# Kernel optimization log

Hardware: AMD Instinct MI355X
Metric: run time of the kernel (lower is better)

## Reference

```python
import jax, jax.numpy as jnp
import numpy as np

B = 128          # batch of independent QP instances
N = 512          # n_assets
N_ITERS = 500    # accelerated projected-gradient iterations (converges tightly)
POWER_ITERS = 30 # power iterations for Lipschitz estimate


def setup_inputs() -> dict:
    key = jax.random.key(0)
    k1, k2 = jax.random.split(key)
    mu = 0.1 * jax.random.normal(k1, (B, N), dtype=jnp.float32)
    # Sigma must be symmetric PSD for cp.quad_form to define a convex QP
    A = jax.random.normal(k2, (B, N, N), dtype=jnp.float32)
    Sigma = jnp.einsum('bik,bjk->bij', A, A) / N + 1e-3 * jnp.eye(N, dtype=jnp.float32)
    return {"mu": mu, "Sigma": Sigma}


def _project_simplex(v):
    # Euclidean projection of each row of v onto {w : sum w = 1, w >= 0}
    n = v.shape[-1]
    u = jnp.sort(v, axis=-1)[..., ::-1]                    # descending
    css = jnp.cumsum(u, axis=-1) - 1.0
    ind = jnp.arange(1, n + 1, dtype=v.dtype)
    rho = jnp.sum(u - css / ind > 0, axis=-1, keepdims=True)  # >= 1
    theta = jnp.take_along_axis(css, rho - 1, axis=-1) / rho.astype(v.dtype)
    return jnp.maximum(v - theta, 0.0)


def _solve_qp(mu, Sigma):
    # minimize w^T Sigma w - mu^T w  s.t.  sum w = 1, w >= 0
    Sigma = 0.5 * (Sigma + jnp.swapaxes(Sigma, -1, -2))  # quad_form assumes symmetric

    # Lipschitz constant of grad: 2*lambda_max(Sigma), via power iteration
    b = jnp.ones((Sigma.shape[0], Sigma.shape[-1]), dtype=mu.dtype) / Sigma.shape[-1]
    def power_step(b, _):
        Sb = jnp.einsum('bij,bj->bi', Sigma, b)
        b = Sb / (jnp.linalg.norm(Sb, axis=-1, keepdims=True) + 1e-12)
        return b, None
    b, _ = jax.lax.scan(power_step, b, None, length=POWER_ITERS)
    lmax = jnp.einsum('bi,bij,bj->b', b, Sigma, b)[:, None]  # [B,1]
    step = 1.0 / (2.0 * lmax + 1e-8)

    # Accelerated projected gradient (FISTA) on the simplex
    w0 = jnp.ones_like(mu) / mu.shape[-1]
    def fista_step(carry, _):
        w, y, t = carry
        g = 2.0 * jnp.einsum('bij,bj->bi', Sigma, y) - mu
        w_new = _project_simplex(y - step * g)
        t_new = 0.5 * (1.0 + jnp.sqrt(1.0 + 4.0 * t * t))
        y_new = w_new + ((t - 1.0) / t_new) * (w_new - w)
        return (w_new, y_new, t_new), None
    (w, _, _), _ = jax.lax.scan(fista_step, (w0, w0, jnp.float32(1.0)), None, length=N_ITERS)
    return w


def reference(mu, Sigma):
    return _solve_qp(mu, Sigma)
```

## Files before the change

### kernel.cpp

```cpp
#include <hip/hip_runtime.h>
#include <hip/hip_fp16.h>
#include <math.h>

#define BATCH 128
#define NDIM 512
#define NPAIR 256
#define POWER_ITERS 30
#define N_ITERS 500
#define REGK 16
#define LDSP 16
#define STRM 32

typedef _Float16 half2_t __attribute__((ext_vector_type(2)));

union H2x4 { float4 f4; half2_t h[4]; };

__device__ __forceinline__ float4 ld4(const float* p) { return *(const float4*)p; }
__device__ __forceinline__ float4 f4_add(float4 a, float4 b) {
  return make_float4(a.x + b.x, a.y + b.y, a.z + b.z, a.w + b.w);
}
__device__ __forceinline__ float wave_sum64(float x) {
#pragma unroll
  for (int off = 1; off < 64; off <<= 1) x += __shfl_xor(x, off, 64);
  return x;
}
__device__ __forceinline__ float wave_max64(float x) {
#pragma unroll
  for (int off = 1; off < 64; off <<= 1) x = fmaxf(x, __shfl_xor(x, off, 64));
  return x;
}
__device__ __forceinline__ void fd4(float4 sv, half2_t yy,
                                    float& a0, float& a1, float& a2, float& a3) {
  H2x4 s; s.f4 = sv;
  a0 = __builtin_amdgcn_fdot2(s.h[0], yy, a0, false);
  a1 = __builtin_amdgcn_fdot2(s.h[1], yy, a1, false);
  a2 = __builtin_amdgcn_fdot2(s.h[2], yy, a2, false);
  a3 = __builtin_amdgcn_fdot2(s.h[3], yy, a3, false);
}

__global__ void sym_conv_kernel(const float* __restrict__ S, half2_t* __restrict__ Sh) {
  const int bb = blockIdx.x, ti = blockIdx.y, tj = blockIdx.z;
  if (tj < ti) return;
  __shared__ float ta[32][33];
  __shared__ float tb[32][33];
  const float* base = S + (size_t)bb * NDIM * NDIM;
  half2_t* dst = Sh + (size_t)bb * NPAIR * NDIM;
  const int tx = threadIdx.x, ty = threadIdx.y;
#pragma unroll
  for (int k = 0; k < 4; k++) {
    int r = ty + 8 * k;
    ta[r][tx] = base[(size_t)(ti * 32 + r) * NDIM + tj * 32 + tx];
    tb[r][tx] = base[(size_t)(tj * 32 + r) * NDIM + ti * 32 + tx];
  }
  __syncthreads();
#pragma unroll
  for (int k = 0; k < 2; k++) {
    int pi = ty + 8 * k;
    float v0 = 0.5f * (ta[2 * pi][tx] + tb[tx][2 * pi]);
    float v1 = 0.5f * (ta[2 * pi + 1][tx] + tb[tx][2 * pi + 1]);
    half2_t o; o[0] = (_Float16)v0; o[1] = (_Float16)v1;
    dst[(size_t)(ti * 16 + pi) * NDIM + tj * 32 + tx] = o;
  }
  if (ti != tj) {
#pragma unroll
    for (int k = 0; k < 2; k++) {
      int pi = ty + 8 * k;
      float v0 = 0.5f * (tb[2 * pi][tx] + ta[tx][2 * pi]);
      float v1 = 0.5f * (tb[2 * pi + 1][tx] + ta[tx][2 * pi + 1]);
      half2_t o; o[0] = (_Float16)v0; o[1] = (_Float16)v1;
      dst[(size_t)(tj * 16 + pi) * NDIM + ti * 32 + tx] = o;
    }
  }
}

__device__ __forceinline__ void combine_z(const float* __restrict__ zsc, int lane, float* z8) {
#pragma unroll
  for (int q = 0; q < 2; q++) {
    float4 zz = ld4(zsc + 0 * NDIM + 8 * lane + 4 * q);
    zz = f4_add(zz, ld4(zsc + 1 * NDIM + 8 * lane + 4 * q));
    zz = f4_add(zz, ld4(zsc + 2 * NDIM + 8 * lane + 4 * q));
    zz = f4_add(zz, ld4(zsc + 3 * NDIM + 8 * lane + 4 * q));
    z8[4 * q + 0] = zz.x; z8[4 * q + 1] = zz.y;
    z8[4 * q + 2] = zz.z; z8[4 * q + 3] = zz.w;
  }
}

__device__ __forceinline__ void store_y_pairs(half2_t* ysh, int lane, const float* y8) {
  H2x4 yo;
#pragma unroll
  for (int q = 0; q < 4; q++) {
    half2_t v; v[0] = (_Float16)y8[2 * q]; v[1] = (_Float16)y8[2 * q + 1];
    yo.h[q] = v;
  }
  *(float4*)(ysh + 4 * lane) = yo.f4;
}

__global__ __launch_bounds__(512)
void qp_solver_h(const float* __restrict__ mu,
                 const half2_t* __restrict__ Sh,
                 float* __restrict__ out) {
  __shared__ __align__(16) float4 lsm[4 * LDSP][128];
  __shared__ __align__(16) half2_t yh2[NPAIR];
  __shared__ __align__(16) float zsc[4 * NDIM];
  __shared__ int stopf;
  const int tid = threadIdx.x;
  const int g = tid >> 7;
  const int c = tid & 127;
  const int b = blockIdx.x;
  const half2_t* Sb = Sh + (size_t)b * NPAIR * NDIM;
  const float invn = 1.0f / (float)NDIM;
  const half2_t* rp = Sb + (size_t)(64 * g) * NDIM + 4 * c;
  const half2_t* gp = rp + (size_t)(REGK + LDSP) * NDIM;

  float4 sreg[REGK];
#pragma unroll
  for (int p = 0; p < REGK; p++) sreg[p] = *(const float4*)(rp + (size_t)p * NDIM);
#pragma unroll
  for (int k = 0; k < LDSP; k++)
    lsm[g * LDSP + k][c] = *(const float4*)(rp + (size_t)(REGK + k) * NDIM);

  if (tid < NPAIR) { half2_t v; v[0] = (_Float16)invn; v[1] = (_Float16)invn; yh2[tid] = v; }
  if (tid == 0) stopf = 0;

  float y8[8], w8[8];
  float t = 1.0f, step = 0.f, maxinc = 0.f;
  float th = -3e38f;
  if (tid < 64) {
#pragma unroll
    for (int k = 0; k < 8; k++) { y8[k] = invn; w8[k] = invn; }
  }
  __syncthreads();

  const int TOT = POWER_ITERS + 1 + N_ITERS;
  for (int it = 0; it < TOT; it++) {
    float a0 = 0.f, a1 = 0.f, a2 = 0.f, a3 = 0.f;
    {
      const half2_t* ybase = yh2 + 64 * g;
      unsigned m = 0;
#pragma unroll
      for (int j = 0; j < 8; j++) {
        const uint4 u = *(const uint4*)(ybase + REGK + LDSP + 4 * j);
        m |= ((u.x | u.y | u.z | u.w) != 0u ? 1u : 0u) << j;
      }
      float4 stA[4], stB[4];
      if (m & 1u) {
#pragma unroll
        for (int k = 0; k < 4; k++) stA[k] = *(const float4*)(gp + (size_t)(0 + k) * NDIM);
      }
      if (m & 2u) {
#pragma unroll
        for (int k = 0; k < 4; k++) stB[k] = *(const float4*)(gp + (size_t)(4 + k) * NDIM);
      }
#pragma unroll
      for (int ch = 0; ch < REGK / 4; ch++) {
        H2x4 y4; y4.f4 = *(const float4*)(ybase + 4 * ch);
#pragma unroll
        for (int q = 0; q < 4; q++) fd4(sreg[4 * ch + q], y4.h[q], a0, a1, a2, a3);
      }
      if (m & 1u) {
        H2x4 y4; y4.f4 = *(const float4*)(ybase + REGK + LDSP + 0);
#pragma unroll
        for (int k = 0; k < 4; k++) fd4(stA[k], y4.h[k], a0, a1, a2, a3);
      }
      if (m & 4u) {
#pragma unroll
        for (int k = 0; k < 4; k++) stA[k] = *(const float4*)(gp + (size_t)(8 + k) * NDIM);
      }
#pragma unroll
      for (int ch = 0; ch < 2; ch++) {
        H2x4 y4; y4.f4 = *(const float4*)(ybase + REGK + 4 * ch);
#pragma unroll
        for (int q = 0; q < 4; q++)
          fd4(lsm[g * LDSP + 4 * ch + q][c], y4.h[q], a0, a1, a2, a3);
      }
      if (m & 2u) {
        H2x4 y4; y4.f4 = *(const float4*)(ybase + REGK + LDSP + 4);
#pragma unroll
        for (int k = 0; k < 4; k++) fd4(stB[k], y4.h[k], a0, a1, a2, a3);
      }
      if (m & 8u) {
#pragma unroll
        for (int k = 0; k < 4; k++) stB[k] = *(const float4*)(gp + (size_t)(12 + k) * NDIM);
      }
#pragma unroll
      for (int ch = 2; ch < 4; ch++) {
        H2x4 y4; y4.f4 = *(const float4*)(ybase + REGK + 4 * ch);
#pragma unroll
        for (int q = 0; q < 4; q++)
          fd4(lsm[g * LDSP + 4 * ch + q][c], y4.h[q], a0, a1, a2, a3);
      }
      if (m & 4u) {
        H2x4 y4; y4.f4 = *(const float4*)(ybase + REGK + LDSP + 8);
#pragma unroll
        for (int k = 0; k < 4; k++) fd4(stA[k], y4.h[k], a0, a1, a2, a3);
      }
      if (m & 16u) {
#pragma unroll
        for (int k = 0; k < 4; k++) stA[k] = *(const float4*)(gp + (size_t)(16 + k) * NDIM);
      }
      if (m & 8u) {
        H2x4 y4; y4.f4 = *(const float4*)(ybase + REGK + LDSP + 12);
#pragma unroll
        for (int k = 0; k < 4; k++) fd4(stB[k], y4.h[k], a0, a1, a2, a3);
      }
      if (m & 32u) {
#pragma unroll
        for (int k = 0; k < 4; k++) stB[k] = *(const float4*)(gp + (size_t)(20 + k) * NDIM);
      }
      if (m & 16u) {
        H2x4 y4; y4.f4 = *(const float4*)(ybase + REGK + LDSP + 16);
#pragma unroll
        for (int k = 0; k < 4; k++) fd4(stA[k], y4.h[k], a0, a1, a2, a3);
      }
      if (m & 64u) {
#pragma unroll
        for (int k = 0; k < 4; k++) stA[k] = *(const float4*)(gp + (size_t)(24 + k) * NDIM);
      }
      if (m & 32u) {
        H2x4 y4; y4.f4 = *(const float4*)(ybase + REGK + LDSP + 20);
#pragma unroll
        for (int k = 0; k < 4; k++) fd4(stB[k], y4.h[k], a0, a1, a2, a3);
      }
      if (m & 128u) {
#pragma unroll
        for (int k = 0; k < 4; k++) stB[k] = *(const float4*)(gp + (size_t)(28 + k) * NDIM);
      }
      if (m & 64u) {
        H2x4 y4; y4.f4 = *(const float4*)(ybase + REGK + LDSP + 24);
#pragma unroll
        for (int k = 0; k < 4; k++) fd4(stA[k], y4.h[k], a0, a1, a2, a3);
      }
      if (m & 128u) {
        H2x4 y4; y4.f4 = *(const float4*)(ybase + REGK + LDSP + 28);
#pragma unroll
        for (int k = 0; k < 4; k++) fd4(stB[k], y4.h[k], a0, a1, a2, a3);
      }
    }
    *(float4*)(zsc + g * NDIM + 4 * c) = make_float4(a0, a1, a2, a3);
    __syncthreads();

    if (tid < 64) {
      float mu8[8];
      if (it > POWER_ITERS) {
        float4 m0 = ld4(mu + (size_t)b * NDIM + 8 * tid);
        float4 m1 = ld4(mu + (size_t)b * NDIM + 8 * tid + 4);
        mu8[0] = m0.x; mu8[1] = m0.y; mu8[2] = m0.z; mu8[3] = m0.w;
        mu8[4] = m1.x; mu8[5] = m1.y; mu8[6] = m1.z; mu8[7] = m1.w;
      }
      float z8[8];
      combine_z(zsc, tid, z8);
      if (it < POWER_ITERS) {
        float ss = 0.f;
#pragma unroll
        for (int k = 0; k < 8; k++) ss += z8[k] * z8[k];
        ss = wave_sum64(ss);
        float inv = 1.0f / (sqrtf(ss) + 1e-12f);
#pragma unroll
        for (int k = 0; k < 8; k++) y8[k] = z8[k] * inv;
        store_y_pairs(yh2, tid, y8);
      } else if (it == POWER_ITERS) {
        float dd = 0.f;
#pragma unroll
        for (int k = 0; k < 8; k++) dd += z8[k] * y8[k];
        dd = wave_sum64(dd);
        step = 1.0f / (2.0f * dd + 1e-8f);
#pragma unroll
        for (int k = 0; k < 8; k++) { y8[k] = invn; w8[k] = invn; }
        t = 1.0f; maxinc = 0.f;
        store_y_pairs(yh2, tid, y8);
      } else {
        float v8[8];
#pragma unroll
        for (int k = 0; k < 8; k++)
          v8[k] = y8[k] - step * (2.0f * z8[k] - mu8[k]);

        {
          float s = 0.f, cn = 0.f, stot = 0.f;
#pragma unroll
          for (int k = 0; k < 8; k++) {
            stot += v8[k];
            if (v8[k] > th) { s += v8[k]; cn += 1.f; }
          }
#pragma unroll
          for (int off = 1; off < 64; off <<= 1) {
            s    += __shfl_xor(s, off, 64);
            cn   += __shfl_xor(cn, off, 64);
            stot += __shfl_xor(stot, off, 64);
          }
          th = (cn > 0.f) ? (s - 1.0f) / cn
                          : (stot - 1.0f) * (1.0f / 512.0f);
        }
        for (int m2 = 0; m2 < 16; m2++) {
          float s = 0.f, cn = 0.f;
#pragma unroll
          for (int k = 0; k < 8; k++)
            if (v8[k] > th) { s += v8[k]; cn += 1.f; }
#pragma unroll
          for (int off = 1; off < 64; off <<= 1) {
            s  += __shfl_xor(s, off, 64);
            cn += __shfl_xor(cn, off, 64);
          }
          float thn = (s - 1.0f) / cn;
          if (!(thn > th)) break;
          th = thn;
        }

        float tn = 0.5f * (1.0f + sqrtf(1.0f + 4.0f * t * t));
        float coef = (t - 1.0f) / tn;
#pragma unroll
        for (int k = 0; k < 8; k++) {
          float wn = fmaxf(v8[k] - th, 0.0f);
          maxinc = fmaxf(maxinc, fabsf(wn - w8[k]));
          y8[k] = wn + coef * (wn - w8[k]);
          w8[k] = wn;
        }
        t = tn;
        store_y_pairs(yh2, tid, y8);
        if ((it & 3) == 3) {
          float mi = wave_max64(maxinc);
          if (tid == 0) stopf = (mi < 1e-7f) ? (stopf + 1) : 0;
          maxinc = 0.f;
        }
      }
    }
    __syncthreads();
    if (stopf >= 2) break;
  }

  if (tid < 64) {
    *(float4*)(out + (size_t)b * NDIM + 8 * tid)     = make_float4(w8[0], w8[1], w8[2], w8[3]);
    *(float4*)(out + (size_t)b * NDIM + 8 * tid + 4) = make_float4(w8[4], w8[5], w8[6], w8[7]);
  }
}

__global__ void symmetrize_kernel(float* __restrict__ S) {
  const int ti = blockIdx.y, tj = blockIdx.z;
  if (tj < ti) return;
  __shared__ float ta[32][33];
  __shared__ float tb[32][33];
  float* base = S + (size_t)blockIdx.x * NDIM * NDIM;
  const int tx = threadIdx.x, ty = threadIdx.y;
#pragma unroll
  for (int k = 0; k < 4; k++) {
    int r = ty + 8 * k;
    ta[r][tx] = base[(size_t)(ti * 32 + r) * NDIM + tj * 32 + tx];
    tb[r][tx] = base[(size_t)(tj * 32 + r) * NDIM + ti * 32 + tx];
  }
  __syncthreads();
#pragma unroll
  for (int k = 0; k < 4; k++) {
    int r = ty + 8 * k;
    base[(size_t)(ti * 32 + r) * NDIM + tj * 32 + tx] = 0.5f * (ta[r][tx] + tb[tx][r]);
  }
#pragma unroll
  for (int k = 0; k < 4; k++) {
    int r = ty + 8 * k;
    base[(size_t)(tj * 32 + r) * NDIM + ti * 32 + tx] = 0.5f * (tb[r][tx] + ta[tx][r]);
  }
}

__device__ __forceinline__ float4 f4_fma(float4 a, float s, float4 acc) {
  acc.x = fmaf(a.x, s, acc.x); acc.y = fmaf(a.y, s, acc.y);
  acc.z = fmaf(a.z, s, acc.z); acc.w = fmaf(a.w, s, acc.w);
  return acc;
}
__device__ __forceinline__ void matvec_partial(const float* __restrict__ Sb,
                                               const float* __restrict__ yv,
                                               float* __restrict__ zsc, int g, int c) {
  const float* rp = Sb + (size_t)(g * 128) * NDIM + 4 * c;
  const float* yp = yv + g * 128;
  float4 a0 = make_float4(0, 0, 0, 0), a1 = a0, a2 = a0, a3 = a0;
#pragma unroll 4
  for (int m = 0; m < 32; m++) {
    float4 yq = ld4(yp + 4 * m);
    float4 s0 = ld4(rp + (size_t)(4 * m + 0) * NDIM);
    float4 s1 = ld4(rp + (size_t)(4 * m + 1) * NDIM);
    float4 s2 = ld4(rp + (size_t)(4 * m + 2) * NDIM);
    float4 s3 = ld4(rp + (size_t)(4 * m + 3) * NDIM);
    a0 = f4_fma(s0, yq.x, a0); a1 = f4_fma(s1, yq.y, a1);
    a2 = f4_fma(s2, yq.z, a2); a3 = f4_fma(s3, yq.w, a3);
  }
  float4 z = f4_add(f4_add(a0, a1), f4_add(a2, a3));
  *(float4*)(zsc + g * NDIM + 4 * c) = z;
}

__launch_bounds__(512, 1)
__global__ void qp_solver(const float* __restrict__ mu,
                          const float* __restrict__ S,
                          float* __restrict__ out) {
  __shared__ float yv[NDIM];
  __shared__ float zsc[4 * NDIM];
  __shared__ float bc[1];
  const int tid = threadIdx.x, g = tid >> 7, c = tid & 127, b = blockIdx.x;
  const float* Sb = S + (size_t)b * NDIM * NDIM;
  const float invn = 1.0f / (float)NDIM;
  yv[tid] = invn;
  __syncthreads();
  for (int it = 0; it < POWER_ITERS; it++) {
    matvec_partial(Sb, yv, zsc, g, c);
    __syncthreads();
    if (tid < 64) {
      float z8[8]; combine_z(zsc, tid, z8);
      float ss = 0.f;
#pragma unroll
      for (int k = 0; k < 8; k++) ss += z8[k] * z8[k];
      ss = wave_sum64(ss);
      float inv = 1.0f / (sqrtf(ss) + 1e-12f);
      *(float4*)(yv + 8 * tid)     = make_float4(z8[0]*inv, z8[1]*inv, z8[2]*inv, z8[3]*inv);
      *(float4*)(yv + 8 * tid + 4) = make_float4(z8[4]*inv, z8[5]*inv, z8[6]*inv, z8[7]*inv);
    }
    __syncthreads();
  }
  matvec_partial(Sb, yv, zsc, g, c);
  __syncthreads();
  if (tid < 64) {
    float z8[8]; combine_z(zsc, tid, z8);
    float dd = 0.f;
#pragma unroll
    for (int k = 0; k < 8; k++) dd += z8[k] * yv[8 * tid + k];
    dd = wave_sum64(dd);
    if (tid == 0) bc[0] = 1.0f / (2.0f * dd + 1e-8f);
  }
  __syncthreads();
  const float step = bc[0];
  yv[tid] = invn;
  float w8[8], y8[8], mu8[8];
  if (tid < 64) {
#pragma unroll
    for (int k = 0; k < 8; k++) { w8[k] = invn; y8[k] = invn; }
    float4 m0 = ld4(mu + (size_t)b * NDIM + 8 * tid);
    float4 m1 = ld4(mu + (size_t)b * NDIM + 8 * tid + 4);
    mu8[0] = m0.x; mu8[1] = m0.y; mu8[2] = m0.z; mu8[3] = m0.w;
    mu8[4] = m1.x; mu8[5] = m1.y; mu8[6] = m1.z; mu8[7] = m1.w;
  }
  __syncthreads();
  float t = 1.0f;
  for (int it = 0; it < N_ITERS; it++) {
    matvec_partial(Sb, yv, zsc, g, c);
    __syncthreads();
    if (tid < 64) {
      float z8[8], v8[8]; combine_z(zsc, tid, z8);
#pragma unroll
      for (int k = 0; k < 8; k++) v8[k] = y8[k] - step * (2.0f * z8[k] - mu8[k]);
      float th = -1e30f;
      for (int m = 0; m < 64; m++) {
        float s = 0.f, cn = 0.f;
#pragma unroll
        for (int k = 0; k < 8; k++) if (v8[k] > th) { s += v8[k]; cn += 1.f; }
#pragma unroll
        for (int off = 1; off < 64; off <<= 1) { s += __shfl_xor(s, off, 64); cn += __shfl_xor(cn, off, 64); }
        float thn = (s - 1.0f) / cn;
        if (!(thn > th)) break;
        th = thn;
      }
      float tn = 0.5f * (1.0f + sqrtf(1.0f + 4.0f * t * t));
      float coef = (t - 1.0f) / tn;
#pragma unroll
      for (int k = 0; k < 8; k++) {
        float wn = fmaxf(v8[k] - th, 0.0f);
        y8[k] = wn + coef * (wn - w8[k]);
        w8[k] = wn;
      }
      *(float4*)(yv + 8 * tid)     = make_float4(y8[0], y8[1], y8[2], y8[3]);
      *(float4*)(yv + 8 * tid + 4) = make_float4(y8[4], y8[5], y8[6], y8[7]);
      t = tn;
    }
    __syncthreads();
  }
  if (tid < 64) {
    *(float4*)(out + (size_t)b * NDIM + 8 * tid)     = make_float4(w8[0], w8[1], w8[2], w8[3]);
    *(float4*)(out + (size_t)b * NDIM + 8 * tid + 4) = make_float4(w8[4], w8[5], w8[6], w8[7]);
  }
}

extern "C" void kernel_launch(void* const* d_in, const int* in_sizes, int n_in,
                              void* d_out, int out_size, void* d_ws, size_t ws_size,
                              hipStream_t stream) {
  const float* mu = (const float*)d_in[0];
  float* Sg = (float*)d_in[1];
  if (n_in >= 2 && in_sizes[0] > in_sizes[1]) { mu = (const float*)d_in[1]; Sg = (float*)d_in[0]; }
  float* out = (float*)d_out;

  const size_t need = (size_t)BATCH * NPAIR * NDIM * sizeof(half2_t);
  if (ws_size >= need) {
    half2_t* Sh = (half2_t*)d_ws;
    sym_conv_kernel<<<dim3(BATCH, 16, 16), dim3(32, 8), 0, stream>>>(Sg, Sh);
    qp_solver_h<<<dim3(BATCH), dim3(512), 0, stream>>>(mu, Sh, out);
  } else {
    symmetrize_kernel<<<dim3(BATCH, 16, 16), dim3(32, 8), 0, stream>>>(Sg);
    qp_solver<<<dim3(BATCH), dim3(512), 0, stream>>>(mu, Sg, out);
  }
}
```

Before: 1.834 ms.

## Split each QP across two workgroups with global-memory flag handshake

Adds a solver variant that launches two workgroups per batch instance. Each holds half of the fp16 Sigma pairs entirely in registers and LDS, so no per-iteration global streaming of Sigma is needed. The partial matvec results are exchanged through a workspace buffer with release/acquire flags and a spin-wait, and both halves then run the identical projection and FISTA update. This relies on both blocks of a pair being co-resident (256 blocks on the device) and adds a cross-workgroup sync each iteration. The fallback kernel also drops its sparsity-mask skipping of streamed Sigma loads.

```diff
diff --git a/kernel.cpp b/kernel.cpp
--- a/kernel.cpp
+++ b/kernel.cpp
@@ -7,9 +7,10 @@
 #define NPAIR 256
 #define POWER_ITERS 30
 #define N_ITERS 500
+#define SREGK 16
+#define SLDSP 16
 #define REGK 16
 #define LDSP 16
-#define STRM 32
 
 typedef _Float16 half2_t __attribute__((ext_vector_type(2)));
 
@@ -93,6 +94,182 @@
     yo.h[q] = v;
   }
   *(float4*)(ysh + 4 * lane) = yo.f4;
+}
+
+__global__ __launch_bounds__(512)
+void qp_solver_s(const float* __restrict__ mu,
+                 const half2_t* __restrict__ Sh,
+                 float* __restrict__ zx,
+                 unsigned* __restrict__ fl,
+                 float* __restrict__ out) {
+  __shared__ __align__(16) float4 lsm[4 * SLDSP][128];
+  __shared__ __align__(16) half2_t yh2[NPAIR];
+  __shared__ __align__(16) float zsc[4 * NDIM];
+  __shared__ int stopf;
+  const int tid = threadIdx.x;
+  const int g = tid >> 7;
+  const int c = tid & 127;
+  const int bid = blockIdx.x;
+  const int b = bid & 127;
+  const int h = bid >> 7;
+  const half2_t* rp = Sh + (size_t)b * NPAIR * NDIM
+                         + (size_t)(128 * h + 32 * g) * NDIM + 4 * c;
+  float* zmy = zx + ((size_t)b * 2 + h) * NDIM;
+  const float* zpt = zx + ((size_t)b * 2 + (1 - h)) * NDIM;
+  unsigned* fmy = fl + b * 2 + h;
+  const unsigned* fpt = fl + b * 2 + (1 - h);
+  const float invn = 1.0f / (float)NDIM;
+
+  float4 sreg[SREGK];
+#pragma unroll
+  for (int p = 0; p < SREGK; p++) sreg[p] = *(const float4*)(rp + (size_t)p * NDIM);
+#pragma unroll
+  for (int k = 0; k < SLDSP; k++)
+    lsm[g * SLDSP + k][c] = *(const float4*)(rp + (size_t)(SREGK + k) * NDIM);
+
+  if (tid < NPAIR) { half2_t v; v[0] = (_Float16)invn; v[1] = (_Float16)invn; yh2[tid] = v; }
+  if (tid == 0) stopf = 0;
+
+  float y8[8], w8[8];
+  float t = 1.0f, step = 0.f, maxinc = 0.f;
+  float th = -3e38f;
+  if (tid < 64) {
+#pragma unroll
+    for (int k = 0; k < 8; k++) { y8[k] = invn; w8[k] = invn; }
+  }
+  __syncthreads();
+
+  const int TOT = POWER_ITERS + 1 + N_ITERS;
+  for (int it = 0; it < TOT; it++) {
+    float a0 = 0.f, a1 = 0.f, a2 = 0.f, a3 = 0.f;
+    {
+      const half2_t* ybase = yh2 + 128 * h + 32 * g;
+#pragma unroll
+      for (int ch = 0; ch < SREGK / 4; ch++) {
+        H2x4 y4; y4.f4 = *(const float4*)(ybase + 4 * ch);
+#pragma unroll
+        for (int q = 0; q < 4; q++) fd4(sreg[4 * ch + q], y4.h[q], a0, a1, a2, a3);
+      }
+#pragma unroll
+      for (int ch = 0; ch < SLDSP / 4; ch++) {
+        H2x4 y4; y4.f4 = *(const float4*)(ybase + SREGK + 4 * ch);
+#pragma unroll
+        for (int q = 0; q < 4; q++)
+          fd4(lsm[g * SLDSP + 4 * ch + q][c], y4.h[q], a0, a1, a2, a3);
+      }
+    }
+    *(float4*)(zsc + g * NDIM + 4 * c) = make_float4(a0, a1, a2, a3);
+    __syncthreads();
+
+    if (tid < 64) {
+      float mu8[8];
+      if (it > POWER_ITERS) {
+        float4 m0 = ld4(mu + (size_t)b * NDIM + 8 * tid);
+        float4 m1 = ld4(mu + (size_t)b * NDIM + 8 * tid + 4);
+        mu8[0] = m0.x; mu8[1] = m0.y; mu8[2] = m0.z; mu8[3] = m0.w;
+        mu8[4] = m1.x; mu8[5] = m1.y; mu8[6] = m1.z; mu8[7] = m1.w;
+      }
+      float z8[8];
+      combine_z(zsc, tid, z8);
+
+      {
+        const unsigned tk = (unsigned)(it + 1);
+#pragma unroll
+        for (int k = 0; k < 8; k++)
+          __hip_atomic_store(zmy + 8 * tid + k, z8[k],
+                             __ATOMIC_RELAXED, __HIP_MEMORY_SCOPE_AGENT);
+        if (tid == 0)
+          __hip_atomic_store(fmy, tk, __ATOMIC_RELEASE, __HIP_MEMORY_SCOPE_AGENT);
+        while (__hip_atomic_load(fpt, __ATOMIC_ACQUIRE, __HIP_MEMORY_SCOPE_AGENT) < tk)
+          __builtin_amdgcn_s_sleep(1);
+#pragma unroll
+        for (int k = 0; k < 8; k++)
+          z8[k] += __hip_atomic_load(zpt + 8 * tid + k,
+                                     __ATOMIC_RELAXED, __HIP_MEMORY_SCOPE_AGENT);
+      }
+
+      if (it < POWER_ITERS) {
+        float ss = 0.f;
+#pragma unroll
+        for (int k = 0; k < 8; k++) ss += z8[k] * z8[k];
+        ss = wave_sum64(ss);
+        float inv = 1.0f / (sqrtf(ss) + 1e-12f);
+#pragma unroll
+        for (int k = 0; k < 8; k++) y8[k] = z8[k] * inv;
+        store_y_pairs(yh2, tid, y8);
+      } else if (it == POWER_ITERS) {
+        float dd = 0.f;
+#pragma unroll
+        for (int k = 0; k < 8; k++) dd += z8[k] * y8[k];
+        dd = wave_sum64(dd);
+        step = 1.0f / (2.0f * dd + 1e-8f);
+#pragma unroll
+        for (int k = 0; k < 8; k++) { y8[k] = invn; w8[k] = invn; }
+        t = 1.0f; maxinc = 0.f;
+        store_y_pairs(yh2, tid, y8);
+      } else {
+        float v8[8];
+#pragma unroll
+        for (int k = 0; k < 8; k++)
+          v8[k] = y8[k] - step * (2.0f * z8[k] - mu8[k]);
+
+        {
+          float s = 0.f, cn = 0.f, stot = 0.f;
+#pragma unroll
+          for (int k = 0; k < 8; k++) {
+            stot += v8[k];
+            if (v8[k] > th) { s += v8[k]; cn += 1.f; }
+          }
+#pragma unroll
+          for (int off = 1; off < 64; off <<= 1) {
+            s    += __shfl_xor(s, off, 64);
+            cn   += __shfl_xor(cn, off, 64);
+            stot += __shfl_xor(stot, off, 64);
+          }
+          th = (cn > 0.f) ? (s - 1.0f) / cn
+                          : (stot - 1.0f) * (1.0f / 512.0f);
+        }
+        for (int m2 = 0; m2 < 16; m2++) {
+          float s = 0.f, cn = 0.f;
+#pragma unroll
+          for (int k = 0; k < 8; k++)
+            if (v8[k] > th) { s += v8[k]; cn += 1.f; }
+#pragma unroll
+          for (int off = 1; off < 64; off <<= 1) {
+            s  += __shfl_xor(s, off, 64);
+            cn += __shfl_xor(cn, off, 64);
+          }
+          float thn = (s - 1.0f) / cn;
+          if (!(thn > th)) break;
+          th = thn;
+        }
+
+        float tn = 0.5f * (1.0f + sqrtf(1.0f + 4.0f * t * t));
+        float coef = (t - 1.0f) / tn;
+#pragma unroll
+        for (int k = 0; k < 8; k++) {
+          float wn = fmaxf(v8[k] - th, 0.0f);
+          maxinc = fmaxf(maxinc, fabsf(wn - w8[k]));
+          y8[k] = wn + coef * (wn - w8[k]);
+          w8[k] = wn;
+        }
+        t = tn;
+        store_y_pairs(yh2, tid, y8);
+        if ((it & 3) == 3) {
+          float mi = wave_max64(maxinc);
+          if (tid == 0) stopf = (mi < 1e-7f) ? (stopf + 1) : 0;
+          maxinc = 0.f;
+        }
+      }
+    }
+    __syncthreads();
+    if (stopf >= 2) break;
+  }
+
+  if (h == 0 && tid < 64) {
+    *(float4*)(out + (size_t)b * NDIM + 8 * tid)     = make_float4(w8[0], w8[1], w8[2], w8[3]);
+    *(float4*)(out + (size_t)b * NDIM + 8 * tid + 4) = make_float4(w8[4], w8[5], w8[6], w8[7]);
+  }
 }
 
 __global__ __launch_bounds__(512)
@@ -136,36 +313,24 @@
     float a0 = 0.f, a1 = 0.f, a2 = 0.f, a3 = 0.f;
     {
       const half2_t* ybase = yh2 + 64 * g;
-      unsigned m = 0;
-#pragma unroll
-      for (int j = 0; j < 8; j++) {
-        const uint4 u = *(const uint4*)(ybase + REGK + LDSP + 4 * j);
-        m |= ((u.x | u.y | u.z | u.w) != 0u ? 1u : 0u) << j;
-      }
       float4 stA[4], stB[4];
-      if (m & 1u) {
-#pragma unroll
-        for (int k = 0; k < 4; k++) stA[k] = *(const float4*)(gp + (size_t)(0 + k) * NDIM);
-      }
-      if (m & 2u) {
-#pragma unroll
-        for (int k = 0; k < 4; k++) stB[k] = *(const float4*)(gp + (size_t)(4 + k) * NDIM);
-      }
+#pragma unroll
+      for (int k = 0; k < 4; k++) stA[k] = *(const float4*)(gp + (size_t)k * NDIM);
+#pragma unroll
+      for (int k = 0; k < 4; k++) stB[k] = *(const float4*)(gp + (size_t)(4 + k) * NDIM);
 #pragma unroll
       for (int ch = 0; ch < REGK / 4; ch++) {
         H2x4 y4; y4.f4 = *(const float4*)(ybase + 4 * ch);
 #pragma unroll
         for (int q = 0; q < 4; q++) fd4(sreg[4 * ch + q], y4.h[q], a0, a1, a2, a3);
       }
-      if (m & 1u) {
-        H2x4 y4; y4.f4 = *(const float4*)(ybase + REGK + LDSP + 0);
+      {
+        H2x4 y4; y4.f4 = *(const float4*)(ybase + REGK + LDSP);
 #pragma unroll
         for (int k = 0; k < 4; k++) fd4(stA[k], y4.h[k], a0, a1, a2, a3);
       }
-      if (m & 4u) {
-#pragma unroll
-        for (int k = 0; k < 4; k++) stA[k] = *(const float4*)(gp + (size_t)(8 + k) * NDIM);
-      }
+#pragma unroll
+      for (int k = 0; k < 4; k++) stA[k] = *(const float4*)(gp + (size_t)(8 + k) * NDIM);
 #pragma unroll
       for (int ch = 0; ch < 2; ch++) {
         H2x4 y4; y4.f4 = *(const float4*)(ybase + REGK + 4 * ch);
@@ -173,15 +338,13 @@
         for (int q = 0; q < 4; q++)
           fd4(lsm[g * LDSP + 4 * ch + q][c], y4.h[q], a0, a1, a2, a3);
       }
-      if (m & 2u) {
+      {
         H2x4 y4; y4.f4 = *(const float4*)(ybase + REGK + LDSP + 4);
 #pragma unroll
         for (int k = 0; k < 4; k++) fd4(stB[k], y4.h[k], a0, a1, a2, a3);
       }
-      if (m & 8u) {
-#pragma unroll
-        for (int k = 0; k < 4; k++) stB[k] = *(const float4*)(gp + (size_t)(12 + k) * NDIM);
-      }
+#pragma unroll
+      for (int k = 0; k < 4; k++) stB[k] = *(const float4*)(gp + (size_t)(12 + k) * NDIM);
 #pragma unroll
       for (int ch = 2; ch < 4; ch++) {
         H2x4 y4; y4.f4 = *(const float4*)(ybase + REGK + 4 * ch);
@@ -189,48 +352,40 @@
         for (int q = 0; q < 4; q++)
           fd4(lsm[g * LDSP + 4 * ch + q][c], y4.h[q], a0, a1, a2, a3);
       }
-      if (m & 4u) {
+      {
         H2x4 y4; y4.f4 = *(const float4*)(ybase + REGK + LDSP + 8);
 #pragma unroll
         for (int k = 0; k < 4; k++) fd4(stA[k], y4.h[k], a0, a1, a2, a3);
       }
-      if (m & 16u) {
-#pragma unroll
-        for (int k = 0; k < 4; k++) stA[k] = *(const float4*)(gp + (size_t)(16 + k) * NDIM);
-      }
-      if (m & 8u) {
+#pragma unroll
+      for (int k = 0; k < 4; k++) stA[k] = *(const float4*)(gp + (size_t)(16 + k) * NDIM);
+      {
         H2x4 y4; y4.f4 = *(const float4*)(ybase + REGK + LDSP + 12);
 #pragma unroll
         for (int k = 0; k < 4; k++) fd4(stB[k], y4.h[k], a0, a1, a2, a3);
       }
-      if (m & 32u) {
-#pragma unroll
-        for (int k = 0; k < 4; k++) stB[k] = *(const float4*)(gp + (size_t)(20 + k) * NDIM);
-      }
-      if (m & 16u) {
+#pragma unroll
+      for (int k = 0; k < 4; k++) stB[k] = *(const float4*)(gp + (size_t)(20 + k) * NDIM);
+      {
         H2x4 y4; y4.f4 = *(const float4*)(ybase + REGK + LDSP + 16);
 #pragma unroll
         for (int k = 0; k < 4; k++) fd4(stA[k], y4.h[k], a0, a1, a2, a3);
       }
-      if (m & 64u) {
-#pragma unroll
-        for (int k = 0; k < 4; k++) stA[k] = *(const float4*)(gp + (size_t)(24 + k) * NDIM);
-      }
-      if (m & 32u) {
+#pragma unroll
+      for (int k = 0; k < 4; k++) stA[k] = *(const float4*)(gp + (size_t)(24 + k) * NDIM);
+      {
         H2x4 y4; y4.f4 = *(const float4*)(ybase + REGK + LDSP + 20);
 #pragma unroll
         for (int k = 0; k < 4; k++) fd4(stB[k], y4.h[k], a0, a1, a2, a3);
       }
-      if (m & 128u) {
-#pragma unroll
-        for (int k = 0; k < 4; k++) stB[k] = *(const float4*)(gp + (size_t)(28 + k) * NDIM);
-      }
-      if (m & 64u) {
+#pragma unroll
+      for (int k = 0; k < 4; k++) stB[k] = *(const float4*)(gp + (size_t)(28 + k) * NDIM);
+      {
         H2x4 y4; y4.f4 = *(const float4*)(ybase + REGK + LDSP + 24);
 #pragma unroll
         for (int k = 0; k < 4; k++) fd4(stA[k], y4.h[k], a0, a1, a2, a3);
       }
-      if (m & 128u) {
+      {
         H2x4 y4; y4.f4 = *(const float4*)(ybase + REGK + LDSP + 28);
 #pragma unroll
         for (int k = 0; k < 4; k++) fd4(stB[k], y4.h[k], a0, a1, a2, a3);
@@ -273,7 +428,6 @@
 #pragma unroll
         for (int k = 0; k < 8; k++)
           v8[k] = y8[k] - step * (2.0f * z8[k] - mu8[k]);
-
         {
           float s = 0.f, cn = 0.f, stot = 0.f;
 #pragma unroll
@@ -304,7 +458,6 @@
           if (!(thn > th)) break;
           th = thn;
         }
-
         float tn = 0.5f * (1.0f + sqrtf(1.0f + 4.0f * t * t));
         float coef = (t - 1.0f) / tn;
 #pragma unroll
@@ -481,8 +634,18 @@
   if (n_in >= 2 && in_sizes[0] > in_sizes[1]) { mu = (const float*)d_in[1]; Sg = (float*)d_in[0]; }
   float* out = (float*)d_out;
 
-  const size_t need = (size_t)BATCH * NPAIR * NDIM * sizeof(half2_t);
-  if (ws_size >= need) {
+  const size_t SHB = (size_t)BATCH * NPAIR * NDIM * sizeof(half2_t);
+  const size_t ZXB = (size_t)BATCH * 2 * NDIM * sizeof(float);
+  const size_t FLB = (size_t)BATCH * 2 * sizeof(unsigned);
+
+  if (ws_size >= SHB + ZXB + FLB) {
+    half2_t* Sh = (half2_t*)d_ws;
+    float* zx = (float*)((char*)d_ws + SHB);
+    unsigned* fl = (unsigned*)((char*)d_ws + SHB + ZXB);
+    hipMemsetAsync(fl, 0, FLB, stream);
+    sym_conv_kernel<<<dim3(BATCH, 16, 16), dim3(32, 8), 0, stream>>>(Sg, Sh);
+    qp_solver_s<<<dim3(2 * BATCH), dim3(512), 0, stream>>>(mu, Sh, zx, fl, out);
+  } else if (ws_size >= SHB) {
     half2_t* Sh = (half2_t*)d_ws;
     sym_conv_kernel<<<dim3(BATCH, 16, 16), dim3(32, 8), 0, stream>>>(Sg, Sh);
     qp_solver_h<<<dim3(BATCH), dim3(512), 0, stream>>>(mu, Sh, out);
```

New measurement: 4.219 ms. +130.1%, slower.
